# Kernel tuning notes

Measured on AMD Instinct MI355X. Metric: run time of the kernel, lower is better.

## Reference

```python
import jax, jax.numpy as jnp
import numpy as np

B, T, V, E, H, FC, O = 4096, 64, 512, 32, 128, 256, 1024


def setup_inputs() -> dict:
    key = jax.random.key(0)
    ks = jax.random.split(key, 12)
    n = lambda k, shape, sc=1.0: (jax.random.normal(k, shape, jnp.float32) * sc)
    return {
        "message": n(ks[0], (B, T, V), 0.1),
        "W_emb": n(ks[1], (E, V), 0.05),
        "b_emb": n(ks[2], (E,), 0.05),
        "init_emb": n(ks[3], (1, 1, E), 1.0),
        "W_ih": n(ks[4], (3 * H, E), 0.08),
        "W_hh": n(ks[5], (3 * H, H), 0.08),
        "b_ih": n(ks[6], (3 * H,), 0.05),
        "b_hh": n(ks[7], (3 * H,), 0.05),
        "W_fc1": n(ks[8], (FC, H), 0.08),
        "b_fc1": n(ks[9], (FC,), 0.05),
        "W_fc2": n(ks[10], (O, FC), 0.05),
        "b_fc2": n(ks[11], (O,), 0.05),
    }


def reference(message, W_emb, b_emb, init_emb, W_ih, W_hh, b_ih, b_hh,
              W_fc1, b_fc1, W_fc2, b_fc2):
    Bb, Tt, Vv = message.shape
    Hh = W_hh.shape[1]
    # Per-step embedding of the message (torch does this inside the loop;
    # it is a pure per-timestep linear so we batch it once): [B,T,E]
    emb = jnp.einsum('btv,ev->bte', message, W_emb) + b_emb
    # Inputs consumed by the GRU at step t: initial_embedding at t=0,
    # then embedding(message[:, t-1]) for t >= 1. The embedding of the
    # final token is computed in torch but never fed to the GRU.
    x0 = jnp.broadcast_to(init_emb[0], (Bb, init_emb.shape[-1]))  # [B,E]
    xs = jnp.concatenate([x0[:, None, :], emb[:, :Tt - 1, :]], axis=1)  # [B,T,E]
    # Precompute input-side gate pre-activations for all steps: [T,B,3H]
    gi_all = jnp.einsum('bte,ge->tbg', xs, W_ih) + b_ih

    def gru_step(h, gi):
        gh = h @ W_hh.T + b_hh  # [B,3H]
        i_r, i_z, i_n = jnp.split(gi, 3, axis=-1)
        h_r, h_z, h_n = jnp.split(gh, 3, axis=-1)
        r = jax.nn.sigmoid(i_r + h_r)
        z = jax.nn.sigmoid(i_z + h_z)
        nng = jnp.tanh(i_n + r * h_n)
        h_new = (1.0 - z) * nng + z * h
        return h_new, None

    h0 = jnp.zeros((Bb, Hh), message.dtype)
    h_last, _ = jax.lax.scan(gru_step, h0, gi_all)
    hid = jax.nn.elu(h_last @ W_fc1.T + b_fc1)
    return jax.nn.sigmoid(hid @ W_fc2.T + b_fc2)
```

## Files before the change

kernel.cpp:

```cpp
#include <hip/hip_runtime.h>
#include <math.h>

#define B_ 4096
#define T_ 64
#define V_ 512
#define E_ 32
#define H_ 128
#define FC1_ 256
#define O_ 1024

typedef float f32x4 __attribute__((ext_vector_type(4)));
typedef short s16x8 __attribute__((ext_vector_type(8)));
typedef unsigned short u16;

#define MFMA16(a, b, c) __builtin_amdgcn_mfma_f32_16x16x32_bf16(a, b, c, 0, 0, 0)

union Frag { u16 q[8]; unsigned u[4]; s16x8 v; };

__device__ __forceinline__ u16 f2bf(float f) {
    union { float f; unsigned u; } v; v.f = f;
    unsigned r = v.u + 0x7FFFu + ((v.u >> 16) & 1u);
    return (u16)(r >> 16);
}
__device__ __forceinline__ unsigned cvtpk(float lo, float hi) {
    unsigned r;
    asm("v_cvt_pk_bf16_f32 %0, %1, %2" : "=v"(r) : "v"(lo), "v"(hi));
    return r;
}
__device__ __forceinline__ float sigf(float x) { return 1.0f / (1.0f + __expf(-x)); }
__device__ __forceinline__ float tanhfast(float x) {
    return 1.0f - 2.0f / (__expf(2.0f * x) + 1.0f);
}
__device__ __forceinline__ void gll16(const float* gsrc, float* ldst) {
    __builtin_amdgcn_global_load_lds(
        (const __attribute__((address_space(1))) unsigned int*)gsrc,
        (__attribute__((address_space(3))) unsigned int*)ldst,
        16, 0, 0);
}
__device__ __forceinline__ s16x8 gatherB(const float* W, int row, int K, int k0, int lh) {
    const float* p = W + (size_t)row * K + k0 + lh * 8;
    float4 a = *(const float4*)p;
    float4 b = *(const float4*)(p + 4);
    Frag f;
    f.u[0] = cvtpk(a.x, a.y); f.u[1] = cvtpk(a.z, a.w);
    f.u[2] = cvtpk(b.x, b.y); f.u[3] = cvtpk(b.z, b.w);
    return f.v;
}

#define STEP_BARRIER() do {                                        \
    asm volatile("s_waitcnt vmcnt(4) lgkmcnt(0)" ::: "memory");    \
    __builtin_amdgcn_s_barrier();                                  \
    __builtin_amdgcn_sched_barrier(0);                             \
} while (0)
#define LDS_BARRIER() do {                                         \
    asm volatile("s_waitcnt lgkmcnt(0)" ::: "memory");             \
    __builtin_amdgcn_s_barrier();                                  \
} while (0)

__global__ void __launch_bounds__(512, 2) fused_kernel(
    const float* __restrict__ msg,
    const float* __restrict__ Wemb, const float* __restrict__ b_emb,
    const float* __restrict__ init_emb,
    const float* __restrict__ Wih, const float* __restrict__ Whh,
    const float* __restrict__ b_ih, const float* __restrict__ b_hh,
    const float* __restrict__ Wfc1, const float* __restrict__ b_fc1,
    const float* __restrict__ Wfc2, const float* __restrict__ b_fc2,
    float* __restrict__ out) {
    __shared__ float mlds[3][16][516];
    __shared__ u16 hlds[2][16 * 136];
    __shared__ float epart[2][8][576];
    __shared__ u16 xfrag[2][640];
    u16* const hidl = (u16*)&epart[0][0][0];
    const int tid = threadIdx.x, w = tid >> 6, l = tid & 63;
    const int ln = l & 15, lh = l >> 4;
    const int wg = w & 3, wp = w >> 2;
    const int gb = blockIdx.x;

    for (int i = tid; i < 16 * 136; i += 512) hlds[0][i] = 0;
    {
        int fr = tid >> 5, fc = tid & 31;
        xfrag[1][fr * 40 + fc] = f2bf(init_emb[fc]);
    }

#define GLL_COL(C, BUF) do {                                                   \
    _Pragma("unroll")                                                          \
    for (int i_ = 0; i_ < 4; i_++) {                                           \
        int r_ = 2 * w + (i_ >> 1);                                            \
        int h_ = (i_ & 1) * 256;                                               \
        gll16(msg + ((size_t)(gb * 16 + r_) * T_ + (C)) * V_ + h_ + l * 4,     \
              &mlds[BUF][r_][h_]);                                             \
    }                                                                          \
} while (0)

    GLL_COL(0, 0);
    GLL_COL(1, 1);
    GLL_COL(2, 2);

    s16x8 wh[3][4], wi[3], we[2][2];
    float br, bz, bin, bgn;
    {
        #pragma unroll
        for (int g = 0; g < 3; g++) {
            int gt = wg + 4 * wp + 8 * g;
            #pragma unroll
            for (int kc = 0; kc < 4; kc++)
                wh[g][kc] = gatherB(Whh, gt * 16 + ln, 128, kc * 32, lh);
            wi[g] = gatherB(Wih, gt * 16 + ln, 32, 0, lh);
        }
        #pragma unroll
        for (int kk = 0; kk < 2; kk++) {
            we[kk][0] = gatherB(Wemb, ln, 512, (2 * w + kk) * 32, lh);
            we[kk][1] = gatherB(Wemb, 16 + ln, 512, (2 * w + kk) * 32, lh);
        }
        int c = wg * 16 + wp * 64 + ln;
        br  = b_ih[c] + b_hh[c];
        bz  = b_ih[128 + c] + b_hh[128 + c];
        bin = b_ih[256 + c];
        bgn = b_hh[256 + c];
    }
    const float bev = b_emb[tid & 31];
    float hold[4] = {};
    __syncthreads();

#define EMBED_LDS(BUF, PAR) do {                                               \
    f32x4 e0 = {0.f, 0.f, 0.f, 0.f}, e1 = {0.f, 0.f, 0.f, 0.f};                \
    _Pragma("unroll")                                                          \
    for (int kk = 0; kk < 2; kk++) {                                           \
        const float* mp = &mlds[BUF][ln][(2 * w + kk) * 32 + lh * 8];          \
        f32x4 m0 = *(const f32x4*)mp;                                          \
        f32x4 m1 = *(const f32x4*)(mp + 4);                                    \
        Frag fa;                                                               \
        fa.u[0] = cvtpk(m0[0], m0[1]); fa.u[1] = cvtpk(m0[2], m0[3]);          \
        fa.u[2] = cvtpk(m1[0], m1[1]); fa.u[3] = cvtpk(m1[2], m1[3]);          \
        e0 = MFMA16(fa.v, we[kk][0], e0);                                      \
        e1 = MFMA16(fa.v, we[kk][1], e1);                                      \
    }                                                                          \
    _Pragma("unroll")                                                          \
    for (int i = 0; i < 4; i++) {                                              \
        epart[PAR][w][(lh * 4 + i) * 36 + ln]      = e0[i];                    \
        epart[PAR][w][(lh * 4 + i) * 36 + 16 + ln] = e1[i];                    \
    }                                                                          \
} while (0)

    EMBED_LDS(0, 1);
    LDS_BARRIER();

    const int aoff = ln * 136 + lh * 8;
    const int colo = wg * 16 + wp * 64 + ln;
    const int fr = tid >> 5, fc = tid & 31, fo = fr * 36 + fc;

#define GRU_STEP(TT, K, ISSUE, EMB, RED) do {                                  \
    const int t = (TT);                                                        \
    if (ISSUE) GLL_COL(t + 3, (K) % 3);                                        \
    const u16* hb = hlds[(K) & 1];                                             \
    s16x8 af0 = *(const s16x8*)(hb + aoff);                                    \
    s16x8 af1 = *(const s16x8*)(hb + aoff + 32);                               \
    s16x8 af2 = *(const s16x8*)(hb + aoff + 64);                               \
    s16x8 af3 = *(const s16x8*)(hb + aoff + 96);                               \
    s16x8 xc = *(const s16x8*)(&xfrag[((K) + 1) & 1][0] + ln * 40 + lh * 8);   \
    f32x4 ar  = {br, br, br, br};                                              \
    f32x4 az  = {bz, bz, bz, bz};                                              \
    f32x4 agn = {bgn, bgn, bgn, bgn};                                          \
    f32x4 ain = {bin, bin, bin, bin};                                          \
    ar  = MFMA16(xc, wi[0], ar);                                               \
    az  = MFMA16(xc, wi[1], az);                                               \
    ain = MFMA16(xc, wi[2], ain);                                              \
    ar  = MFMA16(af0, wh[0][0], ar);                                           \
    ar  = MFMA16(af1, wh[0][1], ar);                                           \
    ar  = MFMA16(af2, wh[0][2], ar);                                           \
    ar  = MFMA16(af3, wh[0][3], ar);                                           \
    az  = MFMA16(af0, wh[1][0], az);                                           \
    az  = MFMA16(af1, wh[1][1], az);                                           \
    az  = MFMA16(af2, wh[1][2], az);                                           \
    az  = MFMA16(af3, wh[1][3], az);                                           \
    agn = MFMA16(af0, wh[2][0], agn);                                          \
    agn = MFMA16(af1, wh[2][1], agn);                                          \
    agn = MFMA16(af2, wh[2][2], agn);                                          \
    agn = MFMA16(af3, wh[2][3], agn);                                          \
    u16* hw = hlds[((K) + 1) & 1];                                             \
    float hn[4];                                                               \
    _Pragma("unroll")                                                          \
    for (int i = 0; i < 4; i++) {                                              \
        float rg = sigf(ar[i]);                                                \
        float zg = sigf(az[i]);                                                \
        float ng = tanhfast(ain[i] + rg * agn[i]);                             \
        hn[i] = zg * (hold[i] - ng) + ng;                                      \
        hold[i] = hn[i];                                                       \
    }                                                                          \
    {                                                                          \
        unsigned u01 = cvtpk(hn[0], hn[1]);                                    \
        unsigned u23 = cvtpk(hn[2], hn[3]);                                    \
        hw[(lh * 4 + 0) * 136 + colo] = (u16)(u01 & 0xFFFFu);                  \
        hw[(lh * 4 + 1) * 136 + colo] = (u16)(u01 >> 16);                      \
        hw[(lh * 4 + 2) * 136 + colo] = (u16)(u23 & 0xFFFFu);                  \
        hw[(lh * 4 + 3) * 136 + colo] = (u16)(u23 >> 16);                      \
    }                                                                          \
    if (EMB) EMBED_LDS(((K) + 1) % 3, (K) & 1);                                \
    if (RED) {                                                                 \
        const float* eb = &epart[((K) + 1) & 1][0][0];                         \
        float s = eb[fo]           + eb[576 + fo]     + eb[2 * 576 + fo]       \
                + eb[3 * 576 + fo] + eb[4 * 576 + fo] + eb[5 * 576 + fo]       \
                + eb[6 * 576 + fo] + eb[7 * 576 + fo] + bev;                   \
        xfrag[(K) & 1][fr * 40 + fc] = f2bf(s);                                \
    }                                                                          \
    STEP_BARRIER();                                                            \
} while (0)

    for (int tt = 0; tt < 60; tt += 6) {
        GRU_STEP(tt + 0, 0, 1, 1, 1);
        GRU_STEP(tt + 1, 1, 1, 1, 1);
        GRU_STEP(tt + 2, 2, 1, 1, 1);
        GRU_STEP(tt + 3, 3, 1, 1, 1);
        GRU_STEP(tt + 4, 4, 1, 1, 1);
        GRU_STEP(tt + 5, 5, 1, 1, 1);
    }
    GRU_STEP(60, 0, 1, 1, 1);
    GRU_STEP(61, 1, 0, 1, 1);
    GRU_STEP(62, 2, 0, 0, 1);
    GRU_STEP(63, 3, 0, 0, 0);
#undef GRU_STEP
#undef GLL_COL
#undef EMBED_LDS

    const u16* hb = hlds[0];
    s16x8 hf0 = *(const s16x8*)(hb + aoff);
    s16x8 hf1 = *(const s16x8*)(hb + aoff + 32);
    s16x8 hf2 = *(const s16x8*)(hb + aoff + 64);
    s16x8 hf3 = *(const s16x8*)(hb + aoff + 96);
    #pragma unroll
    for (int q = 0; q < 2; q++) {
        int ot = 2 * w + q;
        float b1 = b_fc1[ot * 16 + ln];
        f32x4 a1 = {b1, b1, b1, b1};
        a1 = MFMA16(hf0, gatherB(Wfc1, ot * 16 + ln, 128, 0,  lh), a1);
        a1 = MFMA16(hf1, gatherB(Wfc1, ot * 16 + ln, 128, 32, lh), a1);
        a1 = MFMA16(hf2, gatherB(Wfc1, ot * 16 + ln, 128, 64, lh), a1);
        a1 = MFMA16(hf3, gatherB(Wfc1, ot * 16 + ln, 128, 96, lh), a1);
        #pragma unroll
        for (int i = 0; i < 4; i++) {
            float v = a1[i];
            v = v > 0.0f ? v : (__expf(v) - 1.0f);
            hidl[(lh * 4 + i) * 264 + ot * 16 + ln] = f2bf(v);
        }
    }
    LDS_BARRIER();

    s16x8 hf[8];
    #pragma unroll
    for (int kc = 0; kc < 8; kc++)
        hf[kc] = *(const s16x8*)(hidl + ln * 264 + kc * 32 + lh * 8);
    #pragma unroll
    for (int q = 0; q < 8; q++) {
        int nt = 8 * w + q;
        float b2 = b_fc2[nt * 16 + ln];
        f32x4 a2 = {b2, b2, b2, b2};
        #pragma unroll
        for (int kc = 0; kc < 8; kc++)
            a2 = MFMA16(hf[kc], gatherB(Wfc2, nt * 16 + ln, 256, kc * 32, lh), a2);
        #pragma unroll
        for (int i = 0; i < 4; i++)
            out[(size_t)(gb * 16 + lh * 4 + i) * 1024 + nt * 16 + ln] = sigf(a2[i]);
    }
}

extern "C" void kernel_launch(void* const* d_in, const int* in_sizes, int n_in,
                              void* d_out, int out_size, void* d_ws, size_t ws_size,
                              hipStream_t stream) {
    const float* message  = (const float*)d_in[0];
    const float* W_emb    = (const float*)d_in[1];
    const float* b_emb    = (const float*)d_in[2];
    const float* init_emb = (const float*)d_in[3];
    const float* W_ih     = (const float*)d_in[4];
    const float* W_hh     = (const float*)d_in[5];
    const float* b_ih     = (const float*)d_in[6];
    const float* b_hh     = (const float*)d_in[7];
    const float* W_fc1    = (const float*)d_in[8];
    const float* b_fc1    = (const float*)d_in[9];
    const float* W_fc2    = (const float*)d_in[10];
    const float* b_fc2    = (const float*)d_in[11];
    float* out = (float*)d_out;
    (void)d_ws; (void)ws_size;

    hipLaunchKernelGGL(fused_kernel, dim3(256), dim3(512), 0, stream,
                       message, W_emb, b_emb, init_emb, W_ih, W_hh, b_ih, b_hh,
                       W_fc1, b_fc1, W_fc2, b_fc2, out);
}
```

Before: 163.2 us.

## Stage message prefetch through registers instead of direct global-to-LDS loads

Replaces the async global_load_lds triple-buffered prefetch with a four-deep register-staged pipeline: message columns are loaded into VGPRs four steps ahead and written to a two-slot LDS buffer mid-step. The step barrier no longer waits on vmcnt. This cuts LDS usage and removes the partial vmem wait at each barrier, at the cost of 16 extra f32x4 registers per thread and compiler-inserted waits before the LDS writes. That register cost may hurt occupancy at 512 threads with two blocks per CU.

Measured after the change: 161.3 us. Within noise of the previous version (-1.2%).

```diff
diff --git a/kernel.cpp b/kernel.cpp
--- a/kernel.cpp
+++ b/kernel.cpp
@@ -30,12 +30,6 @@
 __device__ __forceinline__ float sigf(float x) { return 1.0f / (1.0f + __expf(-x)); }
 __device__ __forceinline__ float tanhfast(float x) {
     return 1.0f - 2.0f / (__expf(2.0f * x) + 1.0f);
-}
-__device__ __forceinline__ void gll16(const float* gsrc, float* ldst) {
-    __builtin_amdgcn_global_load_lds(
-        (const __attribute__((address_space(1))) unsigned int*)gsrc,
-        (__attribute__((address_space(3))) unsigned int*)ldst,
-        16, 0, 0);
 }
 __device__ __forceinline__ s16x8 gatherB(const float* W, int row, int K, int k0, int lh) {
     const float* p = W + (size_t)row * K + k0 + lh * 8;
@@ -47,11 +41,6 @@
     return f.v;
 }
 
-#define STEP_BARRIER() do {                                        \
-    asm volatile("s_waitcnt vmcnt(4) lgkmcnt(0)" ::: "memory");    \
-    __builtin_amdgcn_s_barrier();                                  \
-    __builtin_amdgcn_sched_barrier(0);                             \
-} while (0)
 #define LDS_BARRIER() do {                                         \
     asm volatile("s_waitcnt lgkmcnt(0)" ::: "memory");             \
     __builtin_amdgcn_s_barrier();                                  \
@@ -66,7 +55,7 @@
     const float* __restrict__ Wfc1, const float* __restrict__ b_fc1,
     const float* __restrict__ Wfc2, const float* __restrict__ b_fc2,
     float* __restrict__ out) {
-    __shared__ float mlds[3][16][516];
+    __shared__ float mlds[2][16][516];
     __shared__ u16 hlds[2][16 * 136];
     __shared__ float epart[2][8][576];
     __shared__ u16 xfrag[2][640];
@@ -76,25 +65,26 @@
     const int wg = w & 3, wp = w >> 2;
     const int gb = blockIdx.x;
 
-    for (int i = tid; i < 16 * 136; i += 512) hlds[0][i] = 0;
-    {
-        int fr = tid >> 5, fc = tid & 31;
-        xfrag[1][fr * 40 + fc] = f2bf(init_emb[fc]);
-    }
-
-#define GLL_COL(C, BUF) do {                                                   \
+#define LOADCOL(BUF, C) do {                                                   \
     _Pragma("unroll")                                                          \
     for (int i_ = 0; i_ < 4; i_++) {                                           \
         int r_ = 2 * w + (i_ >> 1);                                            \
-        int h_ = (i_ & 1) * 256;                                               \
-        gll16(msg + ((size_t)(gb * 16 + r_) * T_ + (C)) * V_ + h_ + l * 4,     \
-              &mlds[BUF][r_][h_]);                                             \
-    }                                                                          \
-} while (0)
-
-    GLL_COL(0, 0);
-    GLL_COL(1, 1);
-    GLL_COL(2, 2);
+        int o_ = (i_ & 1) * 256 + l * 4;                                       \
+        BUF[i_] = *(const f32x4*)(msg +                                        \
+            ((size_t)(gb * 16 + r_) * T_ + (C)) * V_ + o_);                    \
+    }                                                                          \
+} while (0)
+#define WRITECOL(BUF, MB) do {                                                 \
+    _Pragma("unroll")                                                          \
+    for (int i_ = 0; i_ < 4; i_++) {                                           \
+        int r_ = 2 * w + (i_ >> 1);                                            \
+        int o_ = (i_ & 1) * 256 + l * 4;                                       \
+        *(f32x4*)&mlds[MB][r_][o_] = BUF[i_];                                  \
+    }                                                                          \
+} while (0)
+
+    f32x4 mb0[4], mb1[4], mb2[4], mb3[4];
+    LOADCOL(mb0, 0); LOADCOL(mb1, 1); LOADCOL(mb2, 2); LOADCOL(mb3, 3);
 
     s16x8 wh[3][4], wi[3], we[2][2];
     float br, bz, bin, bgn;
@@ -120,6 +110,14 @@
     }
     const float bev = b_emb[tid & 31];
     float hold[4] = {};
+
+    for (int i = tid; i < 16 * 136; i += 512) hlds[0][i] = 0;
+    {
+        int fr_ = tid >> 5, fc_ = tid & 31;
+        xfrag[1][fr_ * 40 + fc_] = f2bf(init_emb[fc_]);
+    }
+    WRITECOL(mb0, 0);
+    WRITECOL(mb1, 1);
     __syncthreads();
 
 #define EMBED_LDS(BUF, PAR) do {                                               \
@@ -149,9 +147,9 @@
     const int colo = wg * 16 + wp * 64 + ln;
     const int fr = tid >> 5, fc = tid & 31, fo = fr * 36 + fc;
 
-#define GRU_STEP(TT, K, ISSUE, EMB, RED) do {                                  \
+#define GRU_STEP(TT, K, LOADF, WRF, EMBF, REDF, MB_L, MB_W) do {               \
     const int t = (TT);                                                        \
-    if (ISSUE) GLL_COL(t + 3, (K) % 3);                                        \
+    if (LOADF) LOADCOL(MB_L, t + 4);                                           \
     const u16* hb = hlds[(K) & 1];                                             \
     s16x8 af0 = *(const s16x8*)(hb + aoff);                                    \
     s16x8 af1 = *(const s16x8*)(hb + aoff + 32);                               \
@@ -177,6 +175,7 @@
     agn = MFMA16(af1, wh[2][1], agn);                                          \
     agn = MFMA16(af2, wh[2][2], agn);                                          \
     agn = MFMA16(af3, wh[2][3], agn);                                          \
+    if (WRF) WRITECOL(MB_W, (K) & 1);                                          \
     u16* hw = hlds[((K) + 1) & 1];                                             \
     float hn[4];                                                               \
     _Pragma("unroll")                                                          \
@@ -195,31 +194,30 @@
         hw[(lh * 4 + 2) * 136 + colo] = (u16)(u23 & 0xFFFFu);                  \
         hw[(lh * 4 + 3) * 136 + colo] = (u16)(u23 >> 16);                      \
     }                                                                          \
-    if (EMB) EMBED_LDS(((K) + 1) % 3, (K) & 1);                                \
-    if (RED) {                                                                 \
+    if (EMBF) EMBED_LDS(((K) + 1) & 1, (K) & 1);                               \
+    if (REDF) {                                                                \
         const float* eb = &epart[((K) + 1) & 1][0][0];                         \
         float s = eb[fo]           + eb[576 + fo]     + eb[2 * 576 + fo]       \
                 + eb[3 * 576 + fo] + eb[4 * 576 + fo] + eb[5 * 576 + fo]       \
                 + eb[6 * 576 + fo] + eb[7 * 576 + fo] + bev;                   \
         xfrag[(K) & 1][fr * 40 + fc] = f2bf(s);                                \
     }                                                                          \
-    STEP_BARRIER();                                                            \
-} while (0)
-
-    for (int tt = 0; tt < 60; tt += 6) {
-        GRU_STEP(tt + 0, 0, 1, 1, 1);
-        GRU_STEP(tt + 1, 1, 1, 1, 1);
-        GRU_STEP(tt + 2, 2, 1, 1, 1);
-        GRU_STEP(tt + 3, 3, 1, 1, 1);
-        GRU_STEP(tt + 4, 4, 1, 1, 1);
-        GRU_STEP(tt + 5, 5, 1, 1, 1);
-    }
-    GRU_STEP(60, 0, 1, 1, 1);
-    GRU_STEP(61, 1, 0, 1, 1);
-    GRU_STEP(62, 2, 0, 0, 1);
-    GRU_STEP(63, 3, 0, 0, 0);
+    LDS_BARRIER();                                                             \
+} while (0)
+
+    for (int tt = 0; tt < 60; tt += 4) {
+        GRU_STEP(tt + 0, 0, 1, 1, 1, 1, mb0, mb2);
+        GRU_STEP(tt + 1, 1, 1, 1, 1, 1, mb1, mb3);
+        GRU_STEP(tt + 2, 2, 1, 1, 1, 1, mb2, mb0);
+        GRU_STEP(tt + 3, 3, 1, 1, 1, 1, mb3, mb1);
+    }
+    GRU_STEP(60, 0, 0, 1, 1, 1, mb0, mb2);
+    GRU_STEP(61, 1, 0, 1, 1, 1, mb1, mb3);
+    GRU_STEP(62, 2, 0, 0, 1, 1, mb2, mb0);
+    GRU_STEP(63, 3, 0, 0, 0, 0, mb3, mb1);
 #undef GRU_STEP
-#undef GLL_COL
+#undef LOADCOL
+#undef WRITECOL
 #undef EMBED_LDS
 
     const u16* hb = hlds[0];
```
